# Kernel optimization log

Measured on AMD Instinct MI355X. Metric: run time of the kernel, lower is better.

The kernel has to match this reference:

```python
import jax, jax.numpy as jnp
import numpy as np

N = 8192

def setup_inputs() -> dict:
    key = jax.random.key(0)
    k1, k2, k3, k4, k5, k6 = jax.random.split(key, 6)
    return {
        "t": jnp.zeros((), dtype=jnp.float32),
        "state": jax.random.uniform(k1, (3 * N,), dtype=jnp.float32),
        "betas": jax.random.uniform(k2, (N,), dtype=jnp.float32),
        "deltas": jax.random.uniform(k3, (N,), dtype=jnp.float32),
        "cs": jax.random.uniform(k4, (N,), dtype=jnp.float32),
        "ps": jax.random.uniform(k5, (N,), dtype=jnp.float32),
        "ts": jax.random.uniform(k6, (N, N), dtype=jnp.float32) * 0.5,
    }

def reference(t, state, betas, deltas, cs, ps, ts):
    # squared parametrization of all learned params
    T = jnp.square(ts)                      # [N, N]
    diag = jnp.diagonal(T)                  # T[n, n]
    row_sum = jnp.sum(T, axis=1)            # sum over T[n, :]
    # normalization[n] = min(T[n,n] / (sum_k T[n,k] - T[n,n]), 1)
    norm = jnp.minimum(diag / (row_sum - diag), jnp.float32(1.0))

    s = state.reshape(-1, 3)                # [N, 3] -> (U, I, V) per host
    U, I, V = s[:, 0], s[:, 1], s[:, 2]

    b2 = jnp.square(betas)
    d2 = jnp.square(deltas)
    p2 = jnp.square(ps)
    c2 = jnp.square(cs)

    bUV = b2 * U * V
    dU = -bUV
    dI = bUV - d2 * I
    # coupling[n] = sum_{nbr != n} norm[nbr] * T[nbr, n] * V[nbr]
    coupling = (norm * V) @ T - norm * diag * V
    dV = p2 * I - c2 * V - diag + coupling

    return jnp.stack([dU, dI, dV], axis=1).reshape(-1)
```

## Files before the change

### kernel.cpp

```cpp
#include <hip/hip_runtime.h>

#define NN 8192
#define RPB 8
#define NBLK (NN / RPB)
#define SUB 4


__global__ void __launch_bounds__(256, 4)
main_pass(const float* __restrict__ ts,
          const float* __restrict__ state,
          float* __restrict__ wv,
          float* __restrict__ diag,
          float* __restrict__ partial)
{
    __shared__ float acc[NN];
    __shared__ float wrow[SUB];

    const int tid  = threadIdx.x;
    const int lane = tid & 63;
    const int wid  = tid >> 6;

    #pragma unroll
    for (int i = tid; i < NN; i += 256) acc[i] = 0.f;

    const int row0 = blockIdx.x * RPB;

    for (int s = 0; s < RPB / SUB; ++s) {
        const int r = row0 + s * SUB + wid;
        const float* rp = ts + (size_t)r * NN;
        float sum = 0.f;
        const float4* rp4 = (const float4*)rp;
        #pragma unroll 8
        for (int it = 0; it < 32; ++it) {
            float4 v = rp4[lane + it * 64];
            sum += v.x * v.x + v.y * v.y + v.z * v.z + v.w * v.w;
        }
        #pragma unroll
        for (int off = 32; off; off >>= 1) sum += __shfl_down(sum, off);
        if (lane == 0) {
            float d = rp[r]; d *= d;
            const float nrm = fminf(d / (sum - d), 1.0f);
            const float wr  = nrm * state[3 * r + 2];
            wrow[wid] = wr;
            wv[r]     = wr;
            diag[r]   = d;
        }
        __syncthreads();
        const int colBase = wid * 2048;
        for (int rr = 0; rr < SUB; ++rr) {
            const float wr = wrow[rr];
            const float4* rq = (const float4*)(ts + (size_t)(row0 + s * SUB + rr) * NN + colBase);
            #pragma unroll 8
            for (int it = 0; it < 8; ++it) {
                const int idx = lane + it * 64;
                float4 v = rq[idx];
                float4* a = (float4*)&acc[colBase + idx * 4];
                float4 av = *a;
                av.x += wr * v.x * v.x;
                av.y += wr * v.y * v.y;
                av.z += wr * v.z * v.z;
                av.w += wr * v.w * v.w;
                *a = av;
            }
        }
        __syncthreads();
    }
    float* pout = partial + (size_t)blockIdx.x * NN;
    #pragma unroll
    for (int i = tid; i < NN / 4; i += 256)
        ((float4*)pout)[i] = ((const float4*)acc)[i];
}

__global__ void __launch_bounds__(256)
reduce1(const float* __restrict__ partial, float* __restrict__ partial2)
{
    const int col = blockIdx.x * 1024 + threadIdx.x * 4;
    const float* base = partial + (size_t)blockIdx.y * 32 * NN + col;
    float4 acc = {0.f, 0.f, 0.f, 0.f};
    #pragma unroll 8
    for (int k = 0; k < 32; ++k) {
        float4 v = *(const float4*)(base + (size_t)k * NN);
        acc.x += v.x; acc.y += v.y; acc.z += v.z; acc.w += v.w;
    }
    *(float4*)(partial2 + (size_t)blockIdx.y * NN + col) = acc;
}

__global__ void __launch_bounds__(256)
finalize(const float* __restrict__ state,
         const float* __restrict__ betas,
         const float* __restrict__ deltas,
         const float* __restrict__ cs,
         const float* __restrict__ ps,
         const float* __restrict__ wv,
         const float* __restrict__ diag,
         const float* __restrict__ partial2,
         float* __restrict__ out)
{
    const int j = blockIdx.x * 256 + threadIdx.x;
    float coup = 0.f;
    #pragma unroll 8
    for (int k = 0; k < 32; ++k) coup += partial2[(size_t)k * NN + j];
    const float dj = diag[j];
    coup -= wv[j] * dj;

    const float U = state[3 * j + 0];
    const float I = state[3 * j + 1];
    const float V = state[3 * j + 2];
    const float b2 = betas[j] * betas[j];
    const float d2 = deltas[j] * deltas[j];
    const float p2 = ps[j] * ps[j];
    const float c2 = cs[j] * cs[j];
    const float bUV = b2 * U * V;

    out[3 * j + 0] = -bUV;
    out[3 * j + 1] = bUV - d2 * I;
    out[3 * j + 2] = p2 * I - c2 * V - dj + coup;
}

extern "C" void kernel_launch(void* const* d_in, const int* in_sizes, int n_in,
                              void* d_out, int out_size, void* d_ws, size_t ws_size,
                              hipStream_t stream) {
    const float* state  = (const float*)d_in[1];
    const float* betas  = (const float*)d_in[2];
    const float* deltas = (const float*)d_in[3];
    const float* cs     = (const float*)d_in[4];
    const float* ps     = (const float*)d_in[5];
    const float* ts     = (const float*)d_in[6];
    float* out = (float*)d_out;

    float* wv       = (float*)d_ws;
    float* diag     = wv + NN;
    float* partial  = diag + NN;
    float* partial2 = partial + (size_t)NBLK * NN;

    main_pass<<<NBLK, 256, 0, stream>>>(ts, state, wv, diag, partial);
    reduce1<<<dim3(8, 32), 256, 0, stream>>>(partial, partial2);
    finalize<<<NN / 256, 256, 0, stream>>>(state, betas, deltas, cs, ps,
                                           wv, diag, partial2, out);
}
```

Before: 410.1 us.

## Keep ts rows in registers to read each row once and prefetch next

Main pass now loads each ts row once into per-thread registers, uses it for both the row-sum normalization and the weighted column accumulation, and keeps the column accumulators in registers instead of shared memory. The next row is prefetched into registers while the current row is processed. This removes the second global read of every row and the shared-memory read-modify-write traffic, at the cost of higher register use and two block-wide barriers per row.

Result: faster. 377.4 us (-8.0%).

```diff
diff --git a/kernel.cpp b/kernel.cpp
--- a/kernel.cpp
+++ b/kernel.cpp
@@ -3,72 +3,81 @@
 #define NN 8192
 #define RPB 8
 #define NBLK (NN / RPB)
-#define SUB 4
+#define SLICE2 32
 
 
-__global__ void __launch_bounds__(256, 4)
+__global__ void __launch_bounds__(256)
 main_pass(const float* __restrict__ ts,
           const float* __restrict__ state,
           float* __restrict__ wv,
           float* __restrict__ diag,
           float* __restrict__ partial)
 {
-    __shared__ float acc[NN];
-    __shared__ float wrow[SUB];
+    __shared__ float red[4];
+    __shared__ float wbc;
 
     const int tid  = threadIdx.x;
     const int lane = tid & 63;
     const int wid  = tid >> 6;
+    const int row0 = blockIdx.x * RPB;
+
+    float4 acc[8];
+    #pragma unroll
+    for (int k = 0; k < 8; ++k) acc[k] = make_float4(0.f, 0.f, 0.f, 0.f);
+
+    float4 cur[8], nxt[8];
+    {
+        const float4* rp = (const float4*)(ts + (size_t)row0 * NN);
+        #pragma unroll
+        for (int k = 0; k < 8; ++k) cur[k] = rp[tid + k * 256];
+    }
 
     #pragma unroll
-    for (int i = tid; i < NN; i += 256) acc[i] = 0.f;
-
-    const int row0 = blockIdx.x * RPB;
-
-    for (int s = 0; s < RPB / SUB; ++s) {
-        const int r = row0 + s * SUB + wid;
-        const float* rp = ts + (size_t)r * NN;
-        float sum = 0.f;
-        const float4* rp4 = (const float4*)rp;
-        #pragma unroll 8
-        for (int it = 0; it < 32; ++it) {
-            float4 v = rp4[lane + it * 64];
-            sum += v.x * v.x + v.y * v.y + v.z * v.z + v.w * v.w;
+    for (int r = 0; r < RPB; ++r) {
+        const int row = row0 + r;
+        if (r + 1 < RPB) {
+            const float4* np = (const float4*)(ts + (size_t)(row + 1) * NN);
+            #pragma unroll
+            for (int k = 0; k < 8; ++k) nxt[k] = np[tid + k * 256];
+        }
+        float s = 0.f;
+        #pragma unroll
+        for (int k = 0; k < 8; ++k) {
+            float4 v = cur[k];
+            s += v.x * v.x + v.y * v.y + v.z * v.z + v.w * v.w;
         }
         #pragma unroll
-        for (int off = 32; off; off >>= 1) sum += __shfl_down(sum, off);
-        if (lane == 0) {
-            float d = rp[r]; d *= d;
-            const float nrm = fminf(d / (sum - d), 1.0f);
-            const float wr  = nrm * state[3 * r + 2];
-            wrow[wid] = wr;
-            wv[r]     = wr;
-            diag[r]   = d;
+        for (int off = 32; off; off >>= 1) s += __shfl_down(s, off);
+        if (lane == 0) red[wid] = s;
+        __syncthreads();
+        if (tid == 0) {
+            const float total = red[0] + red[1] + red[2] + red[3];
+            float d = ts[(size_t)row * NN + row];
+            d *= d;
+            const float nrm = fminf(d / (total - d), 1.0f);
+            const float wr  = nrm * state[3 * row + 2];
+            wv[row]   = wr;
+            diag[row] = d;
+            wbc = wr;
         }
         __syncthreads();
-        const int colBase = wid * 2048;
-        for (int rr = 0; rr < SUB; ++rr) {
-            const float wr = wrow[rr];
-            const float4* rq = (const float4*)(ts + (size_t)(row0 + s * SUB + rr) * NN + colBase);
-            #pragma unroll 8
-            for (int it = 0; it < 8; ++it) {
-                const int idx = lane + it * 64;
-                float4 v = rq[idx];
-                float4* a = (float4*)&acc[colBase + idx * 4];
-                float4 av = *a;
-                av.x += wr * v.x * v.x;
-                av.y += wr * v.y * v.y;
-                av.z += wr * v.z * v.z;
-                av.w += wr * v.w * v.w;
-                *a = av;
-            }
+        const float wr = wbc;
+        #pragma unroll
+        for (int k = 0; k < 8; ++k) {
+            float4 v = cur[k];
+            acc[k].x += wr * v.x * v.x;
+            acc[k].y += wr * v.y * v.y;
+            acc[k].z += wr * v.z * v.z;
+            acc[k].w += wr * v.w * v.w;
         }
-        __syncthreads();
+        if (r + 1 < RPB) {
+            #pragma unroll
+            for (int k = 0; k < 8; ++k) cur[k] = nxt[k];
+        }
     }
-    float* pout = partial + (size_t)blockIdx.x * NN;
+    float4* po = (float4*)(partial + (size_t)blockIdx.x * NN);
     #pragma unroll
-    for (int i = tid; i < NN / 4; i += 256)
-        ((float4*)pout)[i] = ((const float4*)acc)[i];
+    for (int k = 0; k < 8; ++k) po[tid + k * 256] = acc[k];
 }
 
 __global__ void __launch_bounds__(256)
@@ -99,7 +108,7 @@
     const int j = blockIdx.x * 256 + threadIdx.x;
     float coup = 0.f;
     #pragma unroll 8
-    for (int k = 0; k < 32; ++k) coup += partial2[(size_t)k * NN + j];
+    for (int k = 0; k < SLICE2; ++k) coup += partial2[(size_t)k * NN + j];
     const float dj = diag[j];
     coup -= wv[j] * dj;
 
@@ -134,7 +143,7 @@
     float* partial2 = partial + (size_t)NBLK * NN;
 
     main_pass<<<NBLK, 256, 0, stream>>>(ts, state, wv, diag, partial);
-    reduce1<<<dim3(8, 32), 256, 0, stream>>>(partial, partial2);
+    reduce1<<<dim3(8, SLICE2), 256, 0, stream>>>(partial, partial2);
     finalize<<<NN / 256, 256, 0, stream>>>(state, betas, deltas, cs, ps,
                                            wv, diag, partial2, out);
 }
```
